# Kernel tuning notes

Hardware: AMD Instinct MI355X
Metric: run time of the kernel (lower is better)

Reference implementation:

```python
import jax, jax.numpy as jnp
import numpy as np

# HGT meta: 2 node types (A=0, B=1), 3 relations (src_type, dst_type)
L, T, R = 3, 2, 3
H, D = 1, 64            # PyG HGTConv default heads=1, head_dim = hidden/heads
F = H * D               # hidden_channels = input feature dim = 64
NA = NB = 131072
E = 1_000_000
REL = [(0, 1), (1, 0), (0, 0)]


def setup_inputs() -> dict:
    key = jax.random.key(0)
    ks = jax.random.split(key, 16)
    sc = 1.0 / np.sqrt(F)
    inp = {}
    inp["xA"] = jax.random.normal(ks[0], (NA, F), jnp.float32)
    inp["xB"] = jax.random.normal(ks[1], (NB, F), jnp.float32)
    # K/Q/V projections per (layer, node_type)
    inp["Wk"] = jax.random.normal(ks[2], (L, T, F, F), jnp.float32) * sc
    inp["bk"] = jnp.zeros((L, T, F), jnp.float32)
    inp["Wq"] = jax.random.normal(ks[3], (L, T, F, F), jnp.float32) * sc
    inp["bq"] = jnp.zeros((L, T, F), jnp.float32)
    inp["Wv"] = jax.random.normal(ks[4], (L, T, F, F), jnp.float32) * sc
    inp["bv"] = jnp.zeros((L, T, F), jnp.float32)
    # per (layer, relation, head) attention / message matrices and priority
    inp["a_rel"] = jax.random.normal(ks[5], (L, R, H, D, D), jnp.float32) * sc
    inp["m_rel"] = jax.random.normal(ks[6], (L, R, H, D, D), jnp.float32) * sc
    inp["p_rel"] = jnp.ones((L, R, H), jnp.float32)
    # output projection + skip gate per (layer, node_type)
    inp["Wa"] = jax.random.normal(ks[7], (L, T, F, F), jnp.float32) * sc
    inp["ba"] = jnp.zeros((L, T, F), jnp.float32)
    inp["skip"] = jnp.ones((L, T), jnp.float32)
    # final readout Linear(hidden, 1)
    inp["lin_w"] = jax.random.normal(ks[8], (F, 1), jnp.float32) * sc
    inp["lin_b"] = jnp.zeros((1,), jnp.float32)
    # edge indices: ei[0]=src, ei[1]=dst (NA == NB so one range works)
    inp["ei1"] = jax.random.randint(ks[9], (2, E), 0, NA, jnp.int32)   # A -> B
    inp["ei2"] = jax.random.randint(ks[10], (2, E), 0, NA, jnp.int32)  # B -> A
    inp["ei3"] = jax.random.randint(ks[11], (2, E), 0, NA, jnp.int32)  # A -> A
    return inp


def _hgt_layer(xs, eis, Wk, bk, Wq, bq, Wv, bv, a_rel, m_rel, p_rel, Wa, ba, skip):
    # per-type K/Q/V projections, reshaped to [N, H, D]
    k = [(xs[t] @ Wk[t] + bk[t]).reshape(-1, H, D) for t in range(T)]
    q = [(xs[t] @ Wq[t] + bq[t]).reshape(-1, H, D) for t in range(T)]
    v = [(xs[t] @ Wv[t] + bv[t]).reshape(-1, H, D) for t in range(T)]
    agg = [jnp.zeros((xs[t].shape[0], H, D), xs[t].dtype) for t in range(T)]
    inv_sqrt_d = jnp.asarray(1.0 / np.sqrt(D), xs[0].dtype)
    for r, (s, d) in enumerate(REL):
        src, dst = eis[r][0], eis[r][1]
        n_d = xs[d].shape[0]
        # relation-specific transforms on source nodes, then edge gather
        k_r = jnp.einsum('nhd,hde->nhe', k[s], a_rel[r])
        v_r = jnp.einsum('nhd,hde->nhe', v[s], m_rel[r])
        # attention score per edge per head: (q_dst . k_src) * p_rel / sqrt(D)
        score = jnp.einsum('ehd,ehd->eh', q[d][dst], k_r[src]) * p_rel[r] * inv_sqrt_d
        # segment softmax over incoming edges of each dst node (per edge type)
        mx = jax.ops.segment_max(score, dst, num_segments=n_d)
        ex = jnp.exp(score - mx[dst])
        den = jax.ops.segment_sum(ex, dst, num_segments=n_d)
        alpha = ex / den[dst]                      # [E, H]
        msg = alpha[:, :, None] * v_r[src]         # [E, H, D]
        agg[d] = agg[d] + jax.ops.segment_sum(msg, dst, num_segments=n_d)
    outs = []
    for t in range(T):
        o = jax.nn.gelu(agg[t].reshape(-1, F), approximate=False) @ Wa[t] + ba[t]
        a = jax.nn.sigmoid(skip[t])               # skip gate (out_dim == in_dim)
        outs.append(a * o + (1.0 - a) * xs[t])
    return outs


def reference(xA, xB, Wk, bk, Wq, bq, Wv, bv, a_rel, m_rel, p_rel, Wa, ba, skip,
              lin_w, lin_b, ei1, ei2, ei3):
    xs = [xA, xB]
    eis = [ei1, ei2, ei3]
    for l in range(L):
        xs = _hgt_layer(xs, eis, Wk[l], bk[l], Wq[l], bq[l], Wv[l], bv[l],
                        a_rel[l], m_rel[l], p_rel[l], Wa[l], ba[l], skip[l])
    x = jnp.concatenate(xs, axis=0)               # concat all node types
    pooled = jnp.sum(x, axis=0, keepdims=True)    # global_add_pool, batch=None
    return pooled @ lin_w + lin_b                 # Linear(hidden, 1) -> [1, 1]
```

## Files before the change

kernel.cpp:

```cpp
#include <hip/hip_runtime.h>
#include <cmath>

#define DEV __device__ __forceinline__

typedef __attribute__((ext_vector_type(8))) short short8v;
typedef __attribute__((ext_vector_type(4))) float f32x4;

DEV float atomicAddF(float* p, float v) {
    return unsafeAtomicAdd(p, v);
}

DEV float gelu_exact(float v) {
    return 0.5f * v * (1.f + erff(v * 0.70710678118654752f));
}

DEV unsigned short f32_to_bf16(float f) {
    union { float f; unsigned int u; } x; x.f = f;
    unsigned int r = x.u + 0x7fffu + ((x.u >> 16) & 1u);
    return (unsigned short)(r >> 16);
}

DEV unsigned int f4_to_fp8x4(float a, float b, float c, float d) {
    int r = __builtin_amdgcn_cvt_pk_fp8_f32(a, b, 0, false);
    r = __builtin_amdgcn_cvt_pk_fp8_f32(c, d, r, true);
    return (unsigned int)r;
}

DEV float4 fp8x4_to_f4(unsigned int w) {
    auto lo = __builtin_amdgcn_cvt_pk_f32_fp8(w, false);
    auto hi = __builtin_amdgcn_cvt_pk_f32_fp8(w, true);
    return make_float4(lo[0], lo[1], hi[0], hi[1]);
}

DEV short8v cvt8_bf16(float4 f0, float4 f1) {
    union { unsigned int u[4]; short8v s; } r;
    asm("v_cvt_pk_bf16_f32 %0, %1, %2" : "=v"(r.u[0]) : "v"(f0.x), "v"(f0.y));
    asm("v_cvt_pk_bf16_f32 %0, %1, %2" : "=v"(r.u[1]) : "v"(f0.z), "v"(f0.w));
    asm("v_cvt_pk_bf16_f32 %0, %1, %2" : "=v"(r.u[2]) : "v"(f1.x), "v"(f1.y));
    asm("v_cvt_pk_bf16_f32 %0, %1, %2" : "=v"(r.u[3]) : "v"(f1.z), "v"(f1.w));
    return r.s;
}


struct MatSetB {
    const unsigned short* Wt[3];
    const float* b[3];
    float*       y[3];
    int          mode[3];
    int          n;
};

#define BCAP2 6144
#define SB_TILE 4096
#define PSTR 129

__global__ __launch_bounds__(256) void combine_w_bf16(
    const float* __restrict__ Wk, const float* __restrict__ bk,
    const float* __restrict__ Wv, const float* __restrict__ bv,
    const float* __restrict__ a_rel, const float* __restrict__ m_rel,
    const float* __restrict__ p_rel, unsigned short* __restrict__ CWt,
    float* __restrict__ Cb)
{
    const int r = blockIdx.x, kv = blockIdx.y, l = blockIdx.z;
    const int srcT[3] = {0, 1, 0};
    const int s = srcT[r];
    const float* Wsrc = (kv == 0 ? Wk : Wv) + ((size_t)(l*2 + s)) * 4096;
    const float* bsrc = (kv == 0 ? bk : bv) + ((size_t)(l*2 + s)) * 64;
    const float* A    = (kv == 0 ? a_rel : m_rel) + ((size_t)(l*3 + r)) * 4096;
    const float scale = (kv == 0) ? p_rel[l*3 + r] * 0.125f : 1.f;

    __shared__ float Ws[4096];
    __shared__ float As[4096];
    const int tid = threadIdx.x;
    for (int k = tid; k < 4096; k += 256) { Ws[k] = Wsrc[k]; As[k] = A[k]; }
    __syncthreads();

    unsigned short* out = CWt + ((size_t)(l*6 + r*2 + kv)) * 4096;
    const int j = tid & 63;
    #pragma unroll
    for (int i = 0; i < 16; i++) {
        const int f = (tid >> 6) * 16 + i;
        float acc = 0.f;
        #pragma unroll
        for (int e = 0; e < 64; e++) acc = fmaf(Ws[f*64 + e], As[e*64 + j], acc);
        const int so = (l == 0) ? f : (4*(f & 15) + (f >> 4));
        out[j*64 + so] = f32_to_bf16(acc * scale);
    }
    if (tid < 64) {
        float acc = 0.f;
        for (int e = 0; e < 64; e++) acc = fmaf(bsrc[e], As[e*64 + tid], acc);
        Cb[(size_t)(l*6 + r*2 + kv) * 64 + tid] = acc * scale;
    }
}

__global__ __launch_bounds__(256) void prep_wt(
    const float* __restrict__ Wq, const float* __restrict__ Wa,
    unsigned short* __restrict__ Wqt, unsigned short* __restrict__ Wat)
{
    const int bid = blockIdx.x;
    const float* src; unsigned short* dst; int useSigma;
    if (bid < 6) { src = Wq + (size_t)bid * 4096; dst = Wqt + (size_t)bid * 4096;
                   useSigma = (bid >= 2); }
    else         { src = Wa + (size_t)(bid - 6) * 4096; dst = Wat + (size_t)(bid - 6) * 4096;
                   useSigma = 1; }
    for (int idx = threadIdx.x; idx < 4096; idx += 256) {
        const int c = idx >> 6, s = idx & 63;
        const int k = useSigma ? (16*(s & 3) + (s >> 2)) : s;
        dst[c*64 + s] = f32_to_bf16(src[k*64 + c]);
    }
}

DEV void proj128_body(const float* __restrict__ x, const MatSetB& ms, int bid, int tid)
{
    const int wv  = tid >> 6;
    const int ln  = tid & 63;
    const int j   = ln & 15;
    const int g   = ln >> 4;
    const long long rowb = (long long)bid * 128 + wv * 32;

    short8v A[2][2];
    #pragma unroll
    for (int rg = 0; rg < 2; rg++) {
        const float* xp = x + (rowb + rg*16 + j) * 64 + g*8;
        #pragma unroll
        for (int ks = 0; ks < 2; ks++) {
            const float4 f0 = *(const float4*)(xp + ks*32);
            const float4 f1 = *(const float4*)(xp + ks*32 + 4);
            A[rg][ks] = cvt8_bf16(f0, f1);
        }
    }

    unsigned int kst[2][4];
    for (int m = 0; m < ms.n; m++) {
        short8v B[4][2];
        #pragma unroll
        for (int ct = 0; ct < 4; ct++) {
            const unsigned short* wp = ms.Wt[m] + (ct*16 + j) * 64 + g*8;
            B[ct][0] = *(const short8v*)(wp);
            B[ct][1] = *(const short8v*)(wp + 32);
        }
        f32x4 acc[2][4];
        #pragma unroll
        for (int ct = 0; ct < 4; ct++) {
            const float bm = ms.b[m][ct*16 + j];
            f32x4 bi = {bm, bm, bm, bm};
            acc[0][ct] = bi; acc[1][ct] = bi;
        }
        #pragma unroll
        for (int rg = 0; rg < 2; rg++)
            #pragma unroll
            for (int ct = 0; ct < 4; ct++) {
                acc[rg][ct] = __builtin_amdgcn_mfma_f32_16x16x32_bf16(
                    A[rg][0], B[ct][0], acc[rg][ct], 0, 0, 0);
                acc[rg][ct] = __builtin_amdgcn_mfma_f32_16x16x32_bf16(
                    A[rg][1], B[ct][1], acc[rg][ct], 0, 0, 0);
            }
        const int mode = ms.mode[m];
        if (mode == 0) {
            float* yb = ms.y[m];
            #pragma unroll
            for (int rg = 0; rg < 2; rg++)
                #pragma unroll
                for (int i = 0; i < 4; i++) {
                    const long long node = rowb + rg*16 + g*4 + i;
                    *(float4*)(yb + node*64 + j*4) = make_float4(
                        acc[rg][0][i], acc[rg][1][i], acc[rg][2][i], acc[rg][3][i]);
                }
        } else if (mode == 1) {
            #pragma unroll
            for (int rg = 0; rg < 2; rg++)
                #pragma unroll
                for (int i = 0; i < 4; i++)
                    kst[rg][i] = f4_to_fp8x4(
                        acc[rg][0][i], acc[rg][1][i], acc[rg][2][i], acc[rg][3][i]);
        } else {
            unsigned char* yb = (unsigned char*)ms.y[m];
            #pragma unroll
            for (int rg = 0; rg < 2; rg++)
                #pragma unroll
                for (int i = 0; i < 4; i++) {
                    const long long node = rowb + rg*16 + g*4 + i;
                    uint2 s;
                    s.x = kst[rg][i];
                    s.y = f4_to_fp8x4(
                        acc[rg][0][i], acc[rg][1][i], acc[rg][2][i], acc[rg][3][i]);
                    *(uint2*)(yb + node*128 + j*8) = s;
                }
        }
    }
}

__global__ __launch_bounds__(256) void proj_pair(
    const float* __restrict__ x1, MatSetB ms1, int g1,
    const float* __restrict__ x2, MatSetB ms2)
{
    const int tid = threadIdx.x;
    if ((int)blockIdx.x < g1) proj128_body(x1, ms1, blockIdx.x, tid);
    else                      proj128_body(x2, ms2, blockIdx.x - g1, tid);
}

DEV void proj16_lean(const float* __restrict__ x, const MatSetB& ms, int bid, int tid)
{
    const int wv = tid >> 6;
    const int ln = tid & 63;
    const int j  = ln & 15;
    const int g  = ln >> 4;
    const long long rowb = (long long)bid * 256 + wv * 16;

    short8v A[2];
    {
        const float* xp = x + (rowb + j) * 64 + g*8;
        #pragma unroll
        for (int ks = 0; ks < 2; ks++) {
            const float4 f0 = *(const float4*)(xp + ks*32);
            const float4 f1 = *(const float4*)(xp + ks*32 + 4);
            A[ks] = cvt8_bf16(f0, f1);
        }
    }

    unsigned int kst[4];
    for (int m = 0; m < ms.n; m++) {
        f32x4 acc[4];
        #pragma unroll
        for (int ct = 0; ct < 4; ct++) {
            const float bm = ms.b[m][ct*16 + j];
            acc[ct] = (f32x4){bm, bm, bm, bm};
        }
        #pragma unroll
        for (int ct = 0; ct < 4; ct++) {
            const unsigned short* wp = ms.Wt[m] + (ct*16 + j) * 64 + g*8;
            const short8v B0 = *(const short8v*)(wp);
            const short8v B1 = *(const short8v*)(wp + 32);
            acc[ct] = __builtin_amdgcn_mfma_f32_16x16x32_bf16(A[0], B0, acc[ct], 0, 0, 0);
            acc[ct] = __builtin_amdgcn_mfma_f32_16x16x32_bf16(A[1], B1, acc[ct], 0, 0, 0);
        }
        const int mode = ms.mode[m];
        if (mode == 0) {
            float* yb = ms.y[m];
            #pragma unroll
            for (int i = 0; i < 4; i++) {
                const long long node = rowb + g*4 + i;
                *(float4*)(yb + node*64 + j*4) = make_float4(
                    acc[0][i], acc[1][i], acc[2][i], acc[3][i]);
            }
        } else if (mode == 1) {
            #pragma unroll
            for (int i = 0; i < 4; i++)
                kst[i] = f4_to_fp8x4(acc[0][i], acc[1][i], acc[2][i], acc[3][i]);
        } else {
            unsigned char* yb = (unsigned char*)ms.y[m];
            #pragma unroll
            for (int i = 0; i < 4; i++) {
                const long long node = rowb + g*4 + i;
                uint2 s;
                s.x = kst[i];
                s.y = f4_to_fp8x4(acc[0][i], acc[1][i], acc[2][i], acc[3][i]);
                *(uint2*)(yb + node*128 + j*8) = s;
            }
        }
    }
}

__global__ __launch_bounds__(256) void scatter_bucket(
    const int* __restrict__ ei, int E, int nbuck,
    int* __restrict__ bcur, int2* __restrict__ pairbuf)
{
    __shared__ int  hist[256];
    __shared__ int  lbase[256];
    __shared__ int  gbase[256];
    __shared__ int  lcur[256];
    __shared__ int  scanbuf[256];
    __shared__ int2 stage[SB_TILE];
    const int tid = threadIdx.x;
    const int tile0 = blockIdx.x * SB_TILE;

    int2 my[16]; int mb[16];
    #pragma unroll
    for (int i = 0; i < 16; i++) {
        const int e = tile0 + tid + i*256;
        if (e < E) { my[i].x = ei[e]; my[i].y = ei[E + e]; mb[i] = my[i].y >> 9; }
        else mb[i] = -1;
    }
    hist[tid] = 0;
    __syncthreads();
    #pragma unroll
    for (int i = 0; i < 16; i++) if (mb[i] >= 0) atomicAdd(&hist[mb[i]], 1);
    __syncthreads();
    const int c = hist[tid];
    scanbuf[tid] = c;
    __syncthreads();
    for (int off = 1; off < 256; off <<= 1) {
        int add = (tid >= off) ? scanbuf[tid - off] : 0;
        __syncthreads();
        scanbuf[tid] += add;
        __syncthreads();
    }
    lbase[tid] = scanbuf[tid] - c;
    lcur[tid]  = scanbuf[tid] - c;
    if (c > 0 && tid < nbuck) gbase[tid] = atomicAdd(bcur + tid * 16, c);
    __syncthreads();
    #pragma unroll
    for (int i = 0; i < 16; i++) {
        if (mb[i] >= 0) {
            const int p = atomicAdd(&lcur[mb[i]], 1);
            stage[p] = my[i];
        }
    }
    __syncthreads();
    if (c > 0 && tid < nbuck) {
        const int gb = gbase[tid];
        const int lb = lbase[tid];
        int2* dstp = pairbuf + (size_t)tid * BCAP2;
        for (int jj = 0; jj < c; jj++) {
            const int gp = gb + jj;
            if (gp < BCAP2) dstp[gp] = stage[lb + jj];
        }
    }
}

__global__ __launch_bounds__(256) void bucket_csr(
    const int2* __restrict__ pairbuf, const int* __restrict__ bcur,
    int* __restrict__ row_ptr, int* __restrict__ row_end,
    int* __restrict__ col, int n)
{
    const int b   = blockIdx.x;
    const int tid = threadIdx.x;
    __shared__ int lcnt[512];
    __shared__ int lcur[512];
    __shared__ int scanbuf[256];
    int cnt = bcur[b * 16];
    if (cnt > BCAP2) cnt = BCAP2;
    lcnt[tid] = 0; lcnt[tid + 256] = 0;
    __syncthreads();
    const int2* src = pairbuf + (size_t)b * BCAP2;
    for (int i = tid; i < cnt; i += 256)
        atomicAdd(&lcnt[src[i].y & 511], 1);
    __syncthreads();
    const int c0 = lcnt[2*tid], c1 = lcnt[2*tid + 1];
    const int s = c0 + c1;
    scanbuf[tid] = s;
    __syncthreads();
    for (int off = 1; off < 256; off <<= 1) {
        int add = (tid >= off) ? scanbuf[tid - off] : 0;
        __syncthreads();
        scanbuf[tid] += add;
        __syncthreads();
    }
    const int excl = scanbuf[tid] - s;
    const int base = b * BCAP2;
    const int d0 = (b << 9) + 2*tid;
    if (d0 < n)     { row_ptr[d0]   = base + excl;      row_end[d0]   = base + excl + c0; }
    if (d0 + 1 < n) { row_ptr[d0+1] = base + excl + c0; row_end[d0+1] = base + excl + c0 + c1; }
    lcur[2*tid] = excl; lcur[2*tid + 1] = excl + c0;
    __syncthreads();
    for (int i = tid; i < cnt; i += 256) {
        const int2 p = src[i];
        const int pos = atomicAdd(&lcur[p.y & 511], 1);
        col[base + pos] = p.x;
    }
}

#define PROC_EDGE(KVR)                                                                 \
    {                                                                                  \
        const float4 ka_ = fp8x4_to_f4(KVR.x);                                         \
        const float4 kb2_ = fp8x4_to_f4(KVR.z);                                        \
        float sc_ = q0.x*ka_.x + q0.y*ka_.y + q0.z*ka_.z + q0.w*ka_.w                  \
                  + q1.x*kb2_.x + q1.y*kb2_.y + q1.z*kb2_.z + q1.w*kb2_.w;             \
        sc_ += __shfl_xor(sc_, 1); sc_ += __shfl_xor(sc_, 2); sc_ += __shfl_xor(sc_, 4);\
        const float p_ = __expf(sc_);                                                  \
        const float4 va_ = fp8x4_to_f4(KVR.y);                                         \
        const float4 vb_ = fp8x4_to_f4(KVR.w);                                         \
        ssum_ += p_;                                                                   \
        acc0_.x = fmaf(p_, va_.x, acc0_.x); acc0_.y = fmaf(p_, va_.y, acc0_.y);        \
        acc0_.z = fmaf(p_, va_.z, acc0_.z); acc0_.w = fmaf(p_, va_.w, acc0_.w);        \
        acc1_.x = fmaf(p_, vb_.x, acc1_.x); acc1_.y = fmaf(p_, vb_.y, acc1_.y);        \
        acc1_.z = fmaf(p_, vb_.z, acc1_.z); acc1_.w = fmaf(p_, vb_.w, acc1_.w);        \
    }

#define AGG_BODY(RP, RE, COL, KV, O0, O1)                                              \
    {                                                                                  \
        float4 acc0_ = {0.f,0.f,0.f,0.f}, acc1_ = {0.f,0.f,0.f,0.f};                   \
        float ssum_ = 0.f;                                                             \
        const int ss0_ = (RP)[dst], ss1_ = (RE)[dst];                                  \
        const unsigned char* kb_ = (KV) + sub*16;                                      \
        int e_ = ss0_;                                                                 \
        uint4 qq0_ = {0,0,0,0}, qq1_ = {0,0,0,0}, qq2_ = {0,0,0,0}, qq3_ = {0,0,0,0};  \
        if (e_ < ss1_)     qq0_ = *(const uint4*)(kb_ + (size_t)(COL)[e_] * 128);      \
        if (e_ + 1 < ss1_) qq1_ = *(const uint4*)(kb_ + (size_t)(COL)[e_+1] * 128);    \
        if (e_ + 2 < ss1_) qq2_ = *(const uint4*)(kb_ + (size_t)(COL)[e_+2] * 128);    \
        if (e_ + 3 < ss1_) qq3_ = *(const uint4*)(kb_ + (size_t)(COL)[e_+3] * 128);    \
        for (; e_ + 4 < ss1_; e_ += 2) {                                               \
            const int nn0_ = (COL)[e_+4];                                              \
            const int nn1_ = (e_ + 5 < ss1_) ? (COL)[e_+5] : nn0_;                     \
            const uint4 tt0_ = *(const uint4*)(kb_ + (size_t)nn0_ * 128);              \
            const uint4 tt1_ = *(const uint4*)(kb_ + (size_t)nn1_ * 128);              \
            PROC_EDGE(qq0_)                                                            \
            PROC_EDGE(qq1_)                                                            \
            qq0_ = qq2_; qq1_ = qq3_; qq2_ = tt0_; qq3_ = tt1_;                        \
        }                                                                              \
        if (e_ < ss1_)     PROC_EDGE(qq0_)                                             \
        if (e_ + 1 < ss1_) PROC_EDGE(qq1_)                                             \
        if (e_ + 2 < ss1_) PROC_EDGE(qq2_)                                             \
        if (e_ + 3 < ss1_) PROC_EDGE(qq3_)                                             \
        const float inv_ = (ssum_ > 0.f) ? 1.f / ssum_ : 0.f;                          \
        O0.x = fmaf(acc0_.x, inv_, O0.x); O0.y = fmaf(acc0_.y, inv_, O0.y);            \
        O0.z = fmaf(acc0_.z, inv_, O0.z); O0.w = fmaf(acc0_.w, inv_, O0.w);            \
        O1.x = fmaf(acc1_.x, inv_, O1.x); O1.y = fmaf(acc1_.y, inv_, O1.y);            \
        O1.z = fmaf(acc1_.z, inv_, O1.z); O1.w = fmaf(acc1_.w, inv_, O1.w);            \
    }

DEV void agg_block(
    const int* __restrict__ rp1, const int* __restrict__ re1, const int* __restrict__ c1,
    const int* __restrict__ rp2, const int* __restrict__ re2, const int* __restrict__ c2,
    const float* __restrict__ q,
    const unsigned char* __restrict__ kva, const unsigned char* __restrict__ kvb,
    float* __restrict__ xio, const unsigned short* __restrict__ Wat,
    const float* __restrict__ ba, const float* __restrict__ skipw,
    int xstd, int dual, int dopool, float* __restrict__ vec,
    int bid, int tid, float* lds, float* lds_pool)
{
    const long long rowb = (long long)bid * 128;
    if (tid < 64) lds_pool[tid] = 0.f;

    {
        const int sub = tid & 7;
        const int dl  = tid >> 3;
        const int dst = (int)rowb + dl;
        const float4* qp = (const float4*)(q + (size_t)dst * 64);
        const float4 q0 = qp[sub*2], q1 = qp[sub*2 + 1];
        float4 o0 = {0.f,0.f,0.f,0.f}, o1 = {0.f,0.f,0.f,0.f};
        AGG_BODY(rp1, re1, c1, kva, o0, o1)
        if (dual) {
            AGG_BODY(rp2, re2, c2, kvb, o0, o1)
        }
        float* lp = lds + (size_t)(8*sub) * PSTR + dl;
        lp[0*PSTR] = gelu_exact(o0.x); lp[1*PSTR] = gelu_exact(o0.y);
        lp[2*PSTR] = gelu_exact(o0.z); lp[3*PSTR] = gelu_exact(o0.w);
        lp[4*PSTR] = gelu_exact(o1.x); lp[5*PSTR] = gelu_exact(o1.y);
        lp[6*PSTR] = gelu_exact(o1.z); lp[7*PSTR] = gelu_exact(o1.w);
    }
    __syncthreads();

    if (tid < 512) {
        const int wv = tid >> 6;
        const int ln = tid & 63;
        const int j  = ln & 15;
        const int g  = ln >> 4;
        const int r  = wv*16 + j;

        short8v A[2];
        #pragma unroll
        for (int ks = 0; ks < 2; ks++) {
            const int pb = g*8 + ks*32;
            const float4 f0 = make_float4(lds[(pb+0)*PSTR + r], lds[(pb+1)*PSTR + r],
                                          lds[(pb+2)*PSTR + r], lds[(pb+3)*PSTR + r]);
            const float4 f1 = make_float4(lds[(pb+4)*PSTR + r], lds[(pb+5)*PSTR + r],
                                          lds[(pb+6)*PSTR + r], lds[(pb+7)*PSTR + r]);
            A[ks] = cvt8_bf16(f0, f1);
        }

        f32x4 acc[4];
        #pragma unroll
        for (int ct = 0; ct < 4; ct++) {
            const float bm = ba[ct*16 + j];
            acc[ct] = (f32x4){bm, bm, bm, bm};
        }
        #pragma unroll
        for (int ct = 0; ct < 4; ct++) {
            const unsigned short* wp = Wat + (ct*16 + j) * 64 + g*8;
            const short8v B0 = *(const short8v*)(wp);
            const short8v B1 = *(const short8v*)(wp + 32);
            acc[ct] = __builtin_amdgcn_mfma_f32_16x16x32_bf16(A[0], B0, acc[ct], 0, 0, 0);
            acc[ct] = __builtin_amdgcn_mfma_f32_16x16x32_bf16(A[1], B1, acc[ct], 0, 0, 0);
        }

        const float gate = 1.f / (1.f + __expf(-skipw[0]));
        const float og   = 1.f - gate;
        float4 pacc = {0.f,0.f,0.f,0.f};
        #pragma unroll
        for (int i = 0; i < 4; i++) {
            const long long node = rowb + wv*16 + g*4 + i;
            float* xp = xio + node*64;
            float4 o;
            if (xstd) {
                o.x = gate*acc[0][i] + og*xp[j];
                o.y = gate*acc[1][i] + og*xp[16 + j];
                o.z = gate*acc[2][i] + og*xp[32 + j];
                o.w = gate*acc[3][i] + og*xp[48 + j];
            } else {
                const float4 xo = *(const float4*)(xp + 4*j);
                o = make_float4(gate*acc[0][i] + og*xo.x,
                                gate*acc[1][i] + og*xo.y,
                                gate*acc[2][i] + og*xo.z,
                                gate*acc[3][i] + og*xo.w);
            }
            if (!dopool) {
                *(float4*)(xp + 4*j) = o;
            } else {
                pacc.x += o.x; pacc.y += o.y; pacc.z += o.z; pacc.w += o.w;
            }
        }
        if (dopool) {
            atomicAdd(&lds_pool[4*j + 0], pacc.x);
            atomicAdd(&lds_pool[4*j + 1], pacc.y);
            atomicAdd(&lds_pool[4*j + 2], pacc.z);
            atomicAdd(&lds_pool[4*j + 3], pacc.w);
        }
    }
    __syncthreads();
    if (dopool && tid < 64) atomicAddF(vec + tid, lds_pool[tid]);
}

__global__ __launch_bounds__(1024, 8) void agg_epilogue(
    const int* __restrict__ rp1, const int* __restrict__ re1, const int* __restrict__ c1,
    const int* __restrict__ rp2, const int* __restrict__ re2, const int* __restrict__ c2,
    const float* __restrict__ q,
    const unsigned char* __restrict__ kva, const unsigned char* __restrict__ kvb,
    float* __restrict__ xio, const unsigned short* __restrict__ Wat,
    const float* __restrict__ ba, const float* __restrict__ skipw,
    int xstd, int dual, int dopool, float* __restrict__ vec)
{
    __shared__ float lds[64 * PSTR];
    __shared__ float lds_pool[64];
    agg_block(rp1, re1, c1, rp2, re2, c2, q, kva, kvb, xio, Wat, ba, skipw,
              xstd, dual, dopool, vec, blockIdx.x, threadIdx.x, lds, lds_pool);
}

__global__ __launch_bounds__(1024, 8) void fused_agg_proj(
    const int* __restrict__ rp, const int* __restrict__ re, const int* __restrict__ colA,
    const float* __restrict__ q, const unsigned char* __restrict__ kv,
    float* __restrict__ xio, const unsigned short* __restrict__ Wat,
    const float* __restrict__ ba, const float* __restrict__ skipw,
    int xstd, int dopool, float* __restrict__ vec, int aggGrid, int projGrid,
    const float* __restrict__ xsrc, MatSetB ms)
{
    __shared__ float lds[64 * PSTR];
    __shared__ float lds_pool[64];
    const int idx = blockIdx.x;
    const int tid = threadIdx.x;
    int isProj, bid;
    if (aggGrid == 2*projGrid) {
        if (idx % 3 == 2) { isProj = 1; bid = idx / 3; }
        else              { isProj = 0; bid = idx - (idx + 1) / 3; }
    } else {
        isProj = (idx >= aggGrid);
        bid = isProj ? idx - aggGrid : idx;
    }
    if (isProj) {
        proj16_lean(xsrc, ms, bid, tid);
    } else {
        agg_block(rp, re, colA, rp, re, colA, q, kv, kv, xio, Wat, ba, skipw,
                  xstd, 0, dopool, vec, bid, tid, lds, lds_pool);
    }
}

__global__ void final_dot(const float* __restrict__ vec, const float* __restrict__ lw,
                          const float* __restrict__ lb, float* __restrict__ out)
{
    const int i = threadIdx.x;
    float v = vec[i] * lw[16*(i & 3) + (i >> 2)];
    #pragma unroll
    for (int m = 32; m >= 1; m >>= 1) v += __shfl_xor(v, m);
    if (i == 0) out[0] = v + lb[0];
}

extern "C" void kernel_launch(void* const* d_in, const int* in_sizes, int n_in,
                              void* d_out, int out_size, void* d_ws, size_t ws_size,
                              hipStream_t stream)
{
    float* xs[2] = {(float*)d_in[0], (float*)d_in[1]};
    const float* Wk    = (const float*)d_in[2];
    const float* bk    = (const float*)d_in[3];
    const float* Wq    = (const float*)d_in[4];
    const float* bq    = (const float*)d_in[5];
    const float* Wv    = (const float*)d_in[6];
    const float* bv    = (const float*)d_in[7];
    const float* a_rel = (const float*)d_in[8];
    const float* m_rel = (const float*)d_in[9];
    const float* p_rel = (const float*)d_in[10];
    const float* Wa    = (const float*)d_in[11];
    const float* ba    = (const float*)d_in[12];
    const float* skipw = (const float*)d_in[13];
    const float* lin_w = (const float*)d_in[14];
    const float* lin_b = (const float*)d_in[15];
    const int*   ei[3] = {(const int*)d_in[16], (const int*)d_in[17], (const int*)d_in[18]};

    const long long NA = in_sizes[0] / 64;
    const long long NB = in_sizes[1] / 64;
    const long long Ns[2] = {NA, NB};
    const long long Nmax = NA > NB ? NA : NB;
    int E[3];
    for (int r = 0; r < 3; r++) E[r] = in_sizes[16 + r] / 2;
    static const int dstN_is_B[3] = {1, 0, 0};
    const long long nbuckMax = (Nmax + 511) >> 9;

    float* w = (float*)d_ws;
    float* qB  = w; w += Nmax * 64;
    float* qA  = w; w += Nmax * 64;
    unsigned char* kv0 = (unsigned char*)w; w += Nmax * 32;
    unsigned char* kv1 = (unsigned char*)w; w += Nmax * 32;
    unsigned char* kv2 = (unsigned char*)w; w += Nmax * 32;
    unsigned short* CWt = (unsigned short*)w; w += 18 * 2048;
    unsigned short* Wqt = (unsigned short*)w; w += 6 * 2048;
    unsigned short* Wat = (unsigned short*)w; w += 6 * 2048;
    float* Cb    = w; w += 18 * 64;
    float* vec   = w; w += 64;
    int* iw = (int*)w;
    int* row_ptr[3]; int* row_end[3]; int* col[3];
    for (int r = 0; r < 3; r++) {
        row_ptr[r] = iw; iw += Nmax;
        row_end[r] = iw; iw += Nmax;
        col[r]     = iw; iw += nbuckMax * BCAP2;
    }
    int*  bcur    = iw; iw += nbuckMax * 16;
    int2* pairbuf = (int2*)iw;

    combine_w_bf16<<<dim3(3, 2, 3), 256, 0, stream>>>(Wk, bk, Wv, bv, a_rel, m_rel, p_rel, CWt, Cb);
    prep_wt<<<12, 256, 0, stream>>>(Wq, Wa, Wqt, Wat);
    hipMemsetAsync(vec, 0, 64 * sizeof(float), stream);

    for (int r = 0; r < 3; r++) {
        const int n = (int)Ns[dstN_is_B[r]];
        const int nbuck = (n + 511) >> 9;
        hipMemsetAsync(bcur, 0, (size_t)nbuck * 16 * sizeof(int), stream);
        scatter_bucket<<<(E[r] + SB_TILE - 1) / SB_TILE, 256, 0, stream>>>(
            ei[r], E[r], nbuck, bcur, pairbuf);
        bucket_csr<<<nbuck, 256, 0, stream>>>(pairbuf, bcur, row_ptr[r], row_end[r], col[r], n);
    }

    const int gA = (int)(NA >> 7), gB = (int)(NB >> 7);
    const int aggB = (int)(NB >> 7);
    const int aggA = (int)(NA >> 7);
    const int prA  = (int)(NA >> 8);
    for (int l = 0; l < 3; l++) {
        const int xstd   = (l == 0) ? 1 : 0;
        const int dopool = (l == 2) ? 1 : 0;
        {
            MatSetB msB; msB.n = 3;
            msB.Wt[0] = Wqt + (size_t)(l*2 + 1) * 4096;  msB.b[0] = bq + (size_t)(l*2 + 1) * 64;
            msB.y[0] = qB;         msB.mode[0] = 0;
            msB.Wt[1] = CWt + (size_t)(l*6 + 2) * 4096;  msB.b[1] = Cb + (size_t)(l*6 + 2) * 64;
            msB.y[1] = nullptr;    msB.mode[1] = 1;
            msB.Wt[2] = CWt + (size_t)(l*6 + 3) * 4096;  msB.b[2] = Cb + (size_t)(l*6 + 3) * 64;
            msB.y[2] = (float*)kv1; msB.mode[2] = 2;
            MatSetB msA; msA.n = 2;
            msA.Wt[0] = CWt + (size_t)(l*6 + 0) * 4096;  msA.b[0] = Cb + (size_t)(l*6 + 0) * 64;
            msA.y[0] = nullptr;    msA.mode[0] = 1;
            msA.Wt[1] = CWt + (size_t)(l*6 + 1) * 4096;  msA.b[1] = Cb + (size_t)(l*6 + 1) * 64;
            msA.y[1] = (float*)kv0; msA.mode[1] = 2;
            msA.Wt[2] = msA.Wt[1]; msA.b[2] = msA.b[1]; msA.y[2] = msA.y[1]; msA.mode[2] = 2;
            proj_pair<<<gB + gA, 256, 0, stream>>>(xs[1], msB, gB, xs[0], msA);
        }
        {
            MatSetB ms2; ms2.n = 3;
            ms2.Wt[0] = Wqt + (size_t)(l*2 + 0) * 4096;  ms2.b[0] = bq + (size_t)(l*2 + 0) * 64;
            ms2.y[0] = qA;         ms2.mode[0] = 0;
            ms2.Wt[1] = CWt + (size_t)(l*6 + 4) * 4096;  ms2.b[1] = Cb + (size_t)(l*6 + 4) * 64;
            ms2.y[1] = nullptr;    ms2.mode[1] = 1;
            ms2.Wt[2] = CWt + (size_t)(l*6 + 5) * 4096;  ms2.b[2] = Cb + (size_t)(l*6 + 5) * 64;
            ms2.y[2] = (float*)kv2; ms2.mode[2] = 2;
            fused_agg_proj<<<aggB + prA, 1024, 0, stream>>>(
                row_ptr[0], row_end[0], col[0], qB, kv0, xs[1],
                Wat + (size_t)(l*2 + 1) * 4096, ba + (size_t)(l*2 + 1) * 64,
                skipw + l*2 + 1, xstd, dopool, vec, aggB, prA, xs[0], ms2);
        }
        agg_epilogue<<<aggA, 1024, 0, stream>>>(
            row_ptr[1], row_end[1], col[1],
            row_ptr[2], row_end[2], col[2],
            qA, kv1, kv2, xs[0],
            Wat + (size_t)(l*2 + 0) * 4096, ba + (size_t)(l*2 + 0) * 64,
            skipw + l*2 + 0, xstd, 1, dopool, vec);
    }

    final_dot<<<1, 64, 0, stream>>>(vec, lin_w, lin_b, (float*)d_out);
}
```

Measured before the change: 828.7 us.

## Merge all projections into one launch and both aggregations into another

Each layer used three launches: paired projections, B-aggregation fused with the A-side q/kv2 projection, then A-aggregation. Now one launch computes all projections, using the wider 128-row projection body for the A q/kv2 set too. A second launch runs both aggregations, interleaving the heavier dual-relation A blocks with the single-relation B blocks. This removes a kernel boundary per layer and improves load balance. The trade-off is that projection work no longer overlaps with aggregation inside a launch.

```diff
diff --git a/kernel.cpp b/kernel.cpp
--- a/kernel.cpp
+++ b/kernel.cpp
@@ -190,75 +190,17 @@
     }
 }
 
-__global__ __launch_bounds__(256) void proj_pair(
+__global__ __launch_bounds__(256) void proj_triple(
     const float* __restrict__ x1, MatSetB ms1, int g1,
-    const float* __restrict__ x2, MatSetB ms2)
+    const float* __restrict__ x2, MatSetB ms2, int g2,
+    const float* __restrict__ x3, MatSetB ms3)
 {
     const int tid = threadIdx.x;
-    if ((int)blockIdx.x < g1) proj128_body(x1, ms1, blockIdx.x, tid);
-    else                      proj128_body(x2, ms2, blockIdx.x - g1, tid);
-}
-
-DEV void proj16_lean(const float* __restrict__ x, const MatSetB& ms, int bid, int tid)
-{
-    const int wv = tid >> 6;
-    const int ln = tid & 63;
-    const int j  = ln & 15;
-    const int g  = ln >> 4;
-    const long long rowb = (long long)bid * 256 + wv * 16;
-
-    short8v A[2];
-    {
-        const float* xp = x + (rowb + j) * 64 + g*8;
-        #pragma unroll
-        for (int ks = 0; ks < 2; ks++) {
-            const float4 f0 = *(const float4*)(xp + ks*32);
-            const float4 f1 = *(const float4*)(xp + ks*32 + 4);
-            A[ks] = cvt8_bf16(f0, f1);
-        }
-    }
-
-    unsigned int kst[4];
-    for (int m = 0; m < ms.n; m++) {
-        f32x4 acc[4];
-        #pragma unroll
-        for (int ct = 0; ct < 4; ct++) {
-            const float bm = ms.b[m][ct*16 + j];
-            acc[ct] = (f32x4){bm, bm, bm, bm};
-        }
-        #pragma unroll
-        for (int ct = 0; ct < 4; ct++) {
-            const unsigned short* wp = ms.Wt[m] + (ct*16 + j) * 64 + g*8;
-            const short8v B0 = *(const short8v*)(wp);
-            const short8v B1 = *(const short8v*)(wp + 32);
-            acc[ct] = __builtin_amdgcn_mfma_f32_16x16x32_bf16(A[0], B0, acc[ct], 0, 0, 0);
-            acc[ct] = __builtin_amdgcn_mfma_f32_16x16x32_bf16(A[1], B1, acc[ct], 0, 0, 0);
-        }
-        const int mode = ms.mode[m];
-        if (mode == 0) {
-            float* yb = ms.y[m];
-            #pragma unroll
-            for (int i = 0; i < 4; i++) {
-                const long long node = rowb + g*4 + i;
-                *(float4*)(yb + node*64 + j*4) = make_float4(
-                    acc[0][i], acc[1][i], acc[2][i], acc[3][i]);
-            }
-        } else if (mode == 1) {
-            #pragma unroll
-            for (int i = 0; i < 4; i++)
-                kst[i] = f4_to_fp8x4(acc[0][i], acc[1][i], acc[2][i], acc[3][i]);
-        } else {
-            unsigned char* yb = (unsigned char*)ms.y[m];
-            #pragma unroll
-            for (int i = 0; i < 4; i++) {
-                const long long node = rowb + g*4 + i;
-                uint2 s;
-                s.x = kst[i];
-                s.y = f4_to_fp8x4(acc[0][i], acc[1][i], acc[2][i], acc[3][i]);
-                *(uint2*)(yb + node*128 + j*8) = s;
-            }
-        }
-    }
+    int idx = blockIdx.x;
+    if (idx < g1) { proj128_body(x1, ms1, idx, tid); return; }
+    idx -= g1;
+    if (idx < g2) { proj128_body(x2, ms2, idx, tid); return; }
+    proj128_body(x3, ms3, idx - g2, tid);
 }
 
 __global__ __launch_bounds__(256) void scatter_bucket(
@@ -511,45 +453,32 @@
     if (dopool && tid < 64) atomicAddF(vec + tid, lds_pool[tid]);
 }
 
-__global__ __launch_bounds__(1024, 8) void agg_epilogue(
+__global__ __launch_bounds__(1024, 8) void agg_all(
+    const int* __restrict__ rp0, const int* __restrict__ re0, const int* __restrict__ c0,
+    const float* __restrict__ qB, const unsigned char* __restrict__ kv0,
+    float* __restrict__ xB, const unsigned short* __restrict__ WatB,
+    const float* __restrict__ baB, const float* __restrict__ skipB,
     const int* __restrict__ rp1, const int* __restrict__ re1, const int* __restrict__ c1,
     const int* __restrict__ rp2, const int* __restrict__ re2, const int* __restrict__ c2,
-    const float* __restrict__ q,
-    const unsigned char* __restrict__ kva, const unsigned char* __restrict__ kvb,
-    float* __restrict__ xio, const unsigned short* __restrict__ Wat,
-    const float* __restrict__ ba, const float* __restrict__ skipw,
-    int xstd, int dual, int dopool, float* __restrict__ vec)
-{
-    __shared__ float lds[64 * PSTR];
-    __shared__ float lds_pool[64];
-    agg_block(rp1, re1, c1, rp2, re2, c2, q, kva, kvb, xio, Wat, ba, skipw,
-              xstd, dual, dopool, vec, blockIdx.x, threadIdx.x, lds, lds_pool);
-}
-
-__global__ __launch_bounds__(1024, 8) void fused_agg_proj(
-    const int* __restrict__ rp, const int* __restrict__ re, const int* __restrict__ colA,
-    const float* __restrict__ q, const unsigned char* __restrict__ kv,
-    float* __restrict__ xio, const unsigned short* __restrict__ Wat,
-    const float* __restrict__ ba, const float* __restrict__ skipw,
-    int xstd, int dopool, float* __restrict__ vec, int aggGrid, int projGrid,
-    const float* __restrict__ xsrc, MatSetB ms)
+    const float* __restrict__ qA, const unsigned char* __restrict__ kv1,
+    const unsigned char* __restrict__ kv2,
+    float* __restrict__ xA, const unsigned short* __restrict__ WatA,
+    const float* __restrict__ baA, const float* __restrict__ skipA,
+    int xstd, int dopool, float* __restrict__ vec, int aggB, int aggA)
 {
     __shared__ float lds[64 * PSTR];
     __shared__ float lds_pool[64];
     const int idx = blockIdx.x;
     const int tid = threadIdx.x;
-    int isProj, bid;
-    if (aggGrid == 2*projGrid) {
-        if (idx % 3 == 2) { isProj = 1; bid = idx / 3; }
-        else              { isProj = 0; bid = idx - (idx + 1) / 3; }
+    const int half = (aggA < aggB) ? aggA : aggB;
+    int isDual, bid;
+    if (idx < 2*half) { isDual = !(idx & 1); bid = idx >> 1; }
+    else              { bid = idx - half;    isDual = (aggA > aggB); }
+    if (isDual) {
+        agg_block(rp1, re1, c1, rp2, re2, c2, qA, kv1, kv2, xA, WatA, baA, skipA,
+                  xstd, 1, dopool, vec, bid, tid, lds, lds_pool);
     } else {
-        isProj = (idx >= aggGrid);
-        bid = isProj ? idx - aggGrid : idx;
-    }
-    if (isProj) {
-        proj16_lean(xsrc, ms, bid, tid);
-    } else {
-        agg_block(rp, re, colA, rp, re, colA, q, kv, kv, xio, Wat, ba, skipw,
+        agg_block(rp0, re0, c0, rp0, re0, c0, qB, kv0, kv0, xB, WatB, baB, skipB,
                   xstd, 0, dopool, vec, bid, tid, lds, lds_pool);
     }
 }
@@ -631,7 +560,6 @@
     const int gA = (int)(NA >> 7), gB = (int)(NB >> 7);
     const int aggB = (int)(NB >> 7);
     const int aggA = (int)(NA >> 7);
-    const int prA  = (int)(NA >> 8);
     for (int l = 0; l < 3; l++) {
         const int xstd   = (l == 0) ? 1 : 0;
         const int dopool = (l == 2) ? 1 : 0;
@@ -649,27 +577,24 @@
             msA.Wt[1] = CWt + (size_t)(l*6 + 1) * 4096;  msA.b[1] = Cb + (size_t)(l*6 + 1) * 64;
             msA.y[1] = (float*)kv0; msA.mode[1] = 2;
             msA.Wt[2] = msA.Wt[1]; msA.b[2] = msA.b[1]; msA.y[2] = msA.y[1]; msA.mode[2] = 2;
-            proj_pair<<<gB + gA, 256, 0, stream>>>(xs[1], msB, gB, xs[0], msA);
-        }
-        {
-            MatSetB ms2; ms2.n = 3;
-            ms2.Wt[0] = Wqt + (size_t)(l*2 + 0) * 4096;  ms2.b[0] = bq + (size_t)(l*2 + 0) * 64;
-            ms2.y[0] = qA;         ms2.mode[0] = 0;
-            ms2.Wt[1] = CWt + (size_t)(l*6 + 4) * 4096;  ms2.b[1] = Cb + (size_t)(l*6 + 4) * 64;
-            ms2.y[1] = nullptr;    ms2.mode[1] = 1;
-            ms2.Wt[2] = CWt + (size_t)(l*6 + 5) * 4096;  ms2.b[2] = Cb + (size_t)(l*6 + 5) * 64;
-            ms2.y[2] = (float*)kv2; ms2.mode[2] = 2;
-            fused_agg_proj<<<aggB + prA, 1024, 0, stream>>>(
-                row_ptr[0], row_end[0], col[0], qB, kv0, xs[1],
-                Wat + (size_t)(l*2 + 1) * 4096, ba + (size_t)(l*2 + 1) * 64,
-                skipw + l*2 + 1, xstd, dopool, vec, aggB, prA, xs[0], ms2);
-        }
-        agg_epilogue<<<aggA, 1024, 0, stream>>>(
+            MatSetB msA2; msA2.n = 3;
+            msA2.Wt[0] = Wqt + (size_t)(l*2 + 0) * 4096;  msA2.b[0] = bq + (size_t)(l*2 + 0) * 64;
+            msA2.y[0] = qA;         msA2.mode[0] = 0;
+            msA2.Wt[1] = CWt + (size_t)(l*6 + 4) * 4096;  msA2.b[1] = Cb + (size_t)(l*6 + 4) * 64;
+            msA2.y[1] = nullptr;    msA2.mode[1] = 1;
+            msA2.Wt[2] = CWt + (size_t)(l*6 + 5) * 4096;  msA2.b[2] = Cb + (size_t)(l*6 + 5) * 64;
+            msA2.y[2] = (float*)kv2; msA2.mode[2] = 2;
+            proj_triple<<<gB + gA + gA, 256, 0, stream>>>(
+                xs[1], msB, gB, xs[0], msA, gA, xs[0], msA2);
+        }
+        agg_all<<<aggB + aggA, 1024, 0, stream>>>(
+            row_ptr[0], row_end[0], col[0], qB, kv0, xs[1],
+            Wat + (size_t)(l*2 + 1) * 4096, ba + (size_t)(l*2 + 1) * 64, skipw + l*2 + 1,
             row_ptr[1], row_end[1], col[1],
             row_ptr[2], row_end[2], col[2],
             qA, kv1, kv2, xs[0],
-            Wat + (size_t)(l*2 + 0) * 4096, ba + (size_t)(l*2 + 0) * 64,
-            skipw + l*2 + 0, xstd, 1, dopool, vec);
+            Wat + (size_t)(l*2 + 0) * 4096, ba + (size_t)(l*2 + 0) * 64, skipw + l*2 + 0,
+            xstd, dopool, vec, aggB, aggA);
     }
 
     final_dot<<<1, 64, 0, stream>>>(vec, lin_w, lin_b, (float*)d_out);
```

Result: no change. 816.1 us (-1.5%).
